# Kernel tuning notes

Measured on AMD Instinct MI355X. Metric: run time of the kernel, lower is better.

Reference implementation:

```python
import jax, jax.numpy as jnp
import numpy as np


def setup_inputs() -> dict:
    key = jax.random.key(0)
    k1, k2, k3 = jax.random.split(key, 3)
    B, C, H, W = 32, 2048, 14, 14
    OUT = 512
    x = jax.random.normal(k1, (B, C, H, W), dtype=jnp.float32)
    gamma = jnp.zeros((1,), dtype=jnp.float32)  # nn.Parameter(torch.zeros(1))
    # 1x1 conv 2048 -> 512 (layer=4 branch), kaiming-ish scale
    conv_w = jax.random.normal(k2, (OUT, C, 1, 1), dtype=jnp.float32) * (1.0 / np.sqrt(C))
    conv_b = jax.random.normal(k3, (OUT,), dtype=jnp.float32) * 0.01
    return {"x": x, "gamma": gamma, "conv_w": conv_w, "conv_b": conv_b}


def reference(x, gamma, conv_w, conv_b):
    B, C, H, W = x.shape
    q = x.reshape(B, C, H * W)                      # [B, C, N]
    # energy[b, c, d] = <q[b,c,:], q[b,d,:]>
    energy = jnp.einsum('bcn,bdn->bcd', q, q)       # [B, C, C]
    # max-subtract trick: softmax(max - energy) along last dim
    energy_new = jnp.max(energy, axis=-1, keepdims=True) - energy
    attention = jax.nn.softmax(energy_new, axis=-1)  # [B, C, C]
    out = jnp.einsum('bcd,bdn->bcn', attention, q).reshape(B, C, H, W)
    out = gamma * out + x
    # 1x1 conv, stride 1, no padding (layer=4 branch)
    pam_out = jax.lax.conv_general_dilated(
        out, conv_w, window_strides=(1, 1), padding='VALID',
        dimension_numbers=('NCHW', 'OIHW', 'NCHW'))
    pam_out = pam_out + conv_b[None, :, None, None]
    return pam_out
```

## Files before the change

kernel.cpp:

```cpp
#include <hip/hip_runtime.h>
#include <hip/hip_bf16.h>
#include <stdint.h>

#define B_   32
#define C_   2048
#define HW_  196
#define OUT_ 512
#define KT_  128
#define MT_  64
#define NKT  (C_ / KT_)

typedef short short8 __attribute__((ext_vector_type(8)));
typedef float floatx4 __attribute__((ext_vector_type(4)));
typedef unsigned short u16;

#define VMCNT_WAIT(n) __builtin_amdgcn_s_waitcnt(0x0F70 | (n))

__device__ __forceinline__ uint32_t pack_bf16(float a, float b) {
  union { __hip_bfloat162 h; uint32_t u; } c;
  c.h = __float22bfloat162_rn(make_float2(a, b));
  return c.u;
}

__device__ __forceinline__ void async_ld16(const u16* g, void* lds_base) {
  __builtin_amdgcn_global_load_lds(
      (const __attribute__((address_space(1))) uint32_t*)g,
      (__attribute__((address_space(3))) uint32_t*)lds_base, 16, 0, 0);
}

__global__ void attn_fallback(const float* __restrict__ x, const float* __restrict__ gamma,
                              float* __restrict__ y) {
  float g = gamma[0];
  if (g == 0.0f) return;
  __shared__ float qc[HW_];
  __shared__ float e[C_];
  __shared__ float red[256];
  int tid = threadIdx.x;
  for (int cRow = blockIdx.x; cRow < C_; cRow += gridDim.x) {
    for (int b = 0; b < B_; ++b) {
      const float* q = x + (size_t)b * C_ * HW_;
      __syncthreads();
      for (int i = tid; i < HW_; i += 256) qc[i] = q[(size_t)cRow * HW_ + i];
      __syncthreads();
      for (int d = tid; d < C_; d += 256) {
        float s = 0.f;
        const float* qd = q + (size_t)d * HW_;
        for (int n = 0; n < HW_; ++n) s += qc[n] * qd[n];
        e[d] = s;
      }
      __syncthreads();
      float mn = 3.4e38f;
      for (int d = tid; d < C_; d += 256) mn = fminf(mn, e[d]);
      red[tid] = mn; __syncthreads();
      for (int s = 128; s > 0; s >>= 1) { if (tid < s) red[tid] = fminf(red[tid], red[tid + s]); __syncthreads(); }
      float emin = red[0];
      __syncthreads();
      float ps = 0.f;
      for (int d = tid; d < C_; d += 256) { float p = __expf(emin - e[d]); e[d] = p; ps += p; }
      red[tid] = ps; __syncthreads();
      for (int s = 128; s > 0; s >>= 1) { if (tid < s) red[tid] += red[tid + s]; __syncthreads(); }
      float S = red[0];
      __syncthreads();
      float invS = 1.f / S;
      for (int n = tid; n < HW_; n += 256) {
        float acc = 0.f;
        for (int d = 0; d < C_; ++d) acc += e[d] * q[(size_t)d * HW_ + n];
        y[((size_t)b * C_ + cRow) * HW_ + n] = g * acc * invS + q[(size_t)cRow * HW_ + n];
      }
    }
  }
}

__global__ __launch_bounds__(256, 3) void xposeW_kernel(
    const float* __restrict__ x, const float* __restrict__ ysrc,
    const float* __restrict__ gamma, u16* __restrict__ xT,
    const float* __restrict__ w, u16* __restrict__ wbf) {
  int tid = threadIdx.x;
  if (blockIdx.x >= 1024) {
    int gid = (blockIdx.x - 1024) * 256 + tid;
    float4 v = ((const float4*)w)[gid];
    ((uint2*)wbf)[gid] = make_uint2(pack_bf16(v.x, v.y), pack_bf16(v.z, v.w));
    return;
  }
  __shared__ float tile[64 * 197];
  const float* src = (gamma[0] != 0.f) ? ysrc : x;
  int b  = blockIdx.x >> 5;
  int c0 = (blockIdx.x & 31) * 64;
  const float* sb = src + ((size_t)b * C_ + c0) * HW_;
  for (int r = 0; r < 13; ++r) {
    int u = r * 256 + tid;
    if (u < 3136) {
      int ci = u / 49, n4 = u - ci * 49;
      float4 v = *(const float4*)(sb + (size_t)ci * HW_ + n4 * 4);
      float* tp = &tile[ci * 197 + n4 * 4];
      tp[0] = v.x; tp[1] = v.y; tp[2] = v.z; tp[3] = v.w;
    }
  }
  __syncthreads();
  u16* xTb = xT + (size_t)b * HW_ * C_ + c0;
  for (int r = 0; r < 7; ++r) {
    int u = r * 256 + tid;
    if (u < 1568) {
      int c8 = u & 7, n = u >> 3;
      const float* tp = &tile[c8 * 8 * 197 + n];
      uint4 o;
      o.x = pack_bf16(tp[0 * 197], tp[1 * 197]);
      o.y = pack_bf16(tp[2 * 197], tp[3 * 197]);
      o.z = pack_bf16(tp[4 * 197], tp[5 * 197]);
      o.w = pack_bf16(tp[6 * 197], tp[7 * 197]);
      *(uint4*)(xTb + (size_t)n * C_ + c8 * 8) = o;
    }
  }
}

template<int P>
__device__ __forceinline__ void gemm_body(
    const u16* __restrict__ xT, const u16* __restrict__ wbf,
    const float* __restrict__ bias, float* __restrict__ out,
    u16* lds0, u16* lds1, int b, int oBase, int n0) {

  int tid  = threadIdx.x;
  int wave = tid >> 6;
  int lane = tid & 63;
  int col  = lane & 15;
  int quad = lane >> 4;

  const u16* xTb  = xT + (size_t)b * HW_ * C_;
  const u16* aPtr = wbf + (size_t)(oBase + wave * 16 + col) * C_;
  int maxRel = HW_ - 1 - n0;

  floatx4 acc[P];
#pragma unroll
  for (int i = 0; i < P; ++i) { floatx4 z = {0.f, 0.f, 0.f, 0.f}; acc[i] = z; }

  const u16* bPtr[P];
  int ldsOff[P];
#pragma unroll
  for (int jj = 0; jj < P; ++jj) {
    int n    = 4 * wave + quad + 16 * jj;
    int srcN = n0 + (n > maxRel ? maxRel : n);
    int kc   = col ^ (4 * wave + quad);
    bPtr[jj]   = xTb + (size_t)srcN * C_ + kc * 8;
    ldsOff[jj] = (wave + 4 * jj) * 512;
  }

  int aK = 0;
  auto issueB = [&](u16* dst) {
#pragma unroll
    for (int jj = 0; jj < P; ++jj) {
      async_ld16(bPtr[jj], dst + ldsOff[jj]);
      bPtr[jj] += KT_;
    }
  };
  uint4 aR[4];
  auto loadA = [&]() {
#pragma unroll
    for (int ks = 0; ks < 4; ++ks)
      aR[ks] = *(const uint4*)(aPtr + aK + ks * 32 + quad * 8);
    aK += KT_;
  };
  auto phase = [&](const u16* buf) {
    __builtin_amdgcn_s_setprio(1);
#pragma unroll
    for (int ks = 0; ks < 4; ++ks) {
      union { uint4 u; short8 v; } af; af.u = aR[ks];
      int chunk = (ks * 4 + quad) ^ col;
      const u16* base = buf + col * KT_ + chunk * 8;
#pragma unroll
      for (int nt = 0; nt < P; ++nt) {
        short8 bf = *(const short8*)(base + nt * 16 * KT_);
        acc[nt] = __builtin_amdgcn_mfma_f32_16x16x32_bf16(af.v, bf, acc[nt], 0, 0, 0);
      }
    }
    __builtin_amdgcn_s_setprio(0);
  };

  issueB(lds0);
  loadA();
  issueB(lds1);
  u16* cur = lds0; u16* nxt = lds1;
#pragma unroll
  for (int kt = 0; kt < NKT - 1; ++kt) {
    VMCNT_WAIT(P);
    __builtin_amdgcn_s_barrier();
    phase(cur);
    loadA();
    __builtin_amdgcn_s_barrier();
    if (kt < NKT - 2) issueB(cur);
    u16* t = cur; cur = nxt; nxt = t;
  }
  VMCNT_WAIT(0);
  __builtin_amdgcn_s_barrier();
  phase(cur);

  int nLim = HW_ - n0; if (nLim > 16 * P) nLim = 16 * P;
  float* outb = out + (size_t)b * OUT_ * HW_;
#pragma unroll
  for (int r = 0; r < 4; ++r) {
    int o = oBase + wave * 16 + quad * 4 + r;
    float bv = bias[o];
    float* orow = outb + (size_t)o * HW_ + n0;
#pragma unroll
    for (int nt = 0; nt < P; ++nt) {
      int nl = nt * 16 + col;
      if (nl < nLim) orow[nl] = acc[nt][r] + bv;
    }
  }
}

__global__ __launch_bounds__(256, 2) void conv_gemm(
    const u16* __restrict__ xT, const u16* __restrict__ wbf,
    const float* __restrict__ bias, float* __restrict__ out) {

  __shared__ __align__(16) u16 Bs2[2][112 * KT_];

  int bid = blockIdx.x;
  int xcd = bid & 7;
  int s   = bid >> 3;
  int ot  = s & 7;
  int g   = ((s >> 3) << 3) | xcd;
  int b   = g >> 1;
  int nh  = g & 1;

  if (nh == 0)
    gemm_body<7>(xT, wbf, bias, out, Bs2[0], Bs2[1], b, ot * MT_, 0);
  else
    gemm_body<6>(xT, wbf, bias, out, Bs2[0], Bs2[1], b, ot * MT_, 112);
}

extern "C" void kernel_launch(void* const* d_in, const int* in_sizes, int n_in,
                              void* d_out, int out_size, void* d_ws, size_t ws_size,
                              hipStream_t stream) {
  const float* x      = (const float*)d_in[0];
  const float* gamma  = (const float*)d_in[1];
  const float* conv_w = (const float*)d_in[2];
  const float* conv_b = (const float*)d_in[3];
  float* out = (float*)d_out;

  const size_t wbf_bytes = (size_t)OUT_ * C_ * sizeof(u16);
  const size_t xT_bytes  = (size_t)B_ * HW_ * C_ * sizeof(u16);
  const size_t y_bytes   = (size_t)B_ * C_ * HW_ * sizeof(float);
  u16*   wbf = (u16*)d_ws;
  u16*   xT  = (u16*)((char*)d_ws + wbf_bytes);
  float* yws = (float*)((char*)d_ws + wbf_bytes + xT_bytes);
  bool have_fallback_ws = ws_size >= wbf_bytes + xT_bytes + y_bytes;
  const float* ysrc = have_fallback_ws ? (const float*)yws : x;

  if (have_fallback_ws)
    attn_fallback<<<dim3(256), dim3(256), 0, stream>>>(x, gamma, yws);
  xposeW_kernel<<<dim3(2048), dim3(256), 0, stream>>>(
      x, ysrc, gamma, xT, conv_w, wbf);
  conv_gemm<<<dim3(512), dim3(256), 0, stream>>>(xT, wbf, conv_b, out);
}
```

Before: 126.2 us.

## Retile conv GEMM to 128 output channels by 64 pixels per block

The 1x1-conv GEMM block tile changes from 64 output channels by 112/84 pixel columns to 128 output channels by 64 pixel columns. Each wave now holds two 16-row A fragments and reuses each LDS B fragment across two MFMAs, which halves LDS reads per MFMA and drops the templated uneven split. The 196 pixels are covered by four 64-wide tiles, the last one overlapping the third. That overlap adds redundant MFMA work and duplicate identical stores, and it raises the A register footprint per wave.

```diff
diff --git a/kernel.cpp b/kernel.cpp
--- a/kernel.cpp
+++ b/kernel.cpp
@@ -7,8 +7,9 @@
 #define HW_  196
 #define OUT_ 512
 #define KT_  128
-#define MT_  64
 #define NKT  (C_ / KT_)
+#define BN_  64
+#define PD_  4
 
 typedef short short8 __attribute__((ext_vector_type(8)));
 typedef float floatx4 __attribute__((ext_vector_type(4)));
@@ -113,11 +114,22 @@
   }
 }
 
-template<int P>
-__device__ __forceinline__ void gemm_body(
+__global__ __launch_bounds__(256, 2) void conv_gemm(
     const u16* __restrict__ xT, const u16* __restrict__ wbf,
-    const float* __restrict__ bias, float* __restrict__ out,
-    u16* lds0, u16* lds1, int b, int oBase, int n0) {
+    const float* __restrict__ bias, float* __restrict__ out) {
+
+  __shared__ __align__(16) u16 Bs2[2][BN_ * KT_];
+
+  int bid = blockIdx.x;
+  int xcd = bid & 7;
+  int s   = bid >> 3;
+  int ot  = s & 3;
+  int gl  = s >> 2;
+  int grp = xcd * 16 + gl;
+  int b   = grp >> 2;
+  int nh  = grp & 3;
+  int n0  = (nh < 3) ? nh * 64 : (HW_ - BN_);
+  int oBase = ot * 128;
 
   int tid  = threadIdx.x;
   int wave = tid >> 6;
@@ -126,62 +138,66 @@
   int quad = lane >> 4;
 
   const u16* xTb  = xT + (size_t)b * HW_ * C_;
-  const u16* aPtr = wbf + (size_t)(oBase + wave * 16 + col) * C_;
-  int maxRel = HW_ - 1 - n0;
-
-  floatx4 acc[P];
-#pragma unroll
-  for (int i = 0; i < P; ++i) { floatx4 z = {0.f, 0.f, 0.f, 0.f}; acc[i] = z; }
-
-  const u16* bPtr[P];
-  int ldsOff[P];
-#pragma unroll
-  for (int jj = 0; jj < P; ++jj) {
-    int n    = 4 * wave + quad + 16 * jj;
-    int srcN = n0 + (n > maxRel ? maxRel : n);
-    int kc   = col ^ (4 * wave + quad);
-    bPtr[jj]   = xTb + (size_t)srcN * C_ + kc * 8;
+  const u16* aPtr = wbf + (size_t)(oBase + wave * 32 + col) * C_ + quad * 8;
+
+  floatx4 acc[2][4];
+#pragma unroll
+  for (int m = 0; m < 2; ++m)
+#pragma unroll
+    for (int nt = 0; nt < 4; ++nt) { floatx4 z = {0.f, 0.f, 0.f, 0.f}; acc[m][nt] = z; }
+
+  const u16* bPtr[PD_];
+  int ldsOff[PD_];
+#pragma unroll
+  for (int jj = 0; jj < PD_; ++jj) {
+    int rl = 4 * wave + quad + 16 * jj;
+    int kc = col ^ (4 * wave + quad);
+    bPtr[jj]   = xTb + (size_t)(n0 + rl) * C_ + kc * 8;
     ldsOff[jj] = (wave + 4 * jj) * 512;
   }
 
+  uint4 aR[8];
   int aK = 0;
+  auto loadA = [&]() {
+#pragma unroll
+    for (int m = 0; m < 2; ++m)
+#pragma unroll
+      for (int ks = 0; ks < 4; ++ks)
+        aR[m * 4 + ks] = *(const uint4*)(aPtr + (size_t)m * 16 * C_ + aK + ks * 32);
+    aK += KT_;
+  };
   auto issueB = [&](u16* dst) {
 #pragma unroll
-    for (int jj = 0; jj < P; ++jj) {
+    for (int jj = 0; jj < PD_; ++jj) {
       async_ld16(bPtr[jj], dst + ldsOff[jj]);
       bPtr[jj] += KT_;
     }
-  };
-  uint4 aR[4];
-  auto loadA = [&]() {
-#pragma unroll
-    for (int ks = 0; ks < 4; ++ks)
-      aR[ks] = *(const uint4*)(aPtr + aK + ks * 32 + quad * 8);
-    aK += KT_;
   };
   auto phase = [&](const u16* buf) {
     __builtin_amdgcn_s_setprio(1);
 #pragma unroll
     for (int ks = 0; ks < 4; ++ks) {
-      union { uint4 u; short8 v; } af; af.u = aR[ks];
+      union { uint4 u; short8 v; } a0, a1;
+      a0.u = aR[ks]; a1.u = aR[4 + ks];
       int chunk = (ks * 4 + quad) ^ col;
       const u16* base = buf + col * KT_ + chunk * 8;
 #pragma unroll
-      for (int nt = 0; nt < P; ++nt) {
+      for (int nt = 0; nt < 4; ++nt) {
         short8 bf = *(const short8*)(base + nt * 16 * KT_);
-        acc[nt] = __builtin_amdgcn_mfma_f32_16x16x32_bf16(af.v, bf, acc[nt], 0, 0, 0);
+        acc[0][nt] = __builtin_amdgcn_mfma_f32_16x16x32_bf16(a0.v, bf, acc[0][nt], 0, 0, 0);
+        acc[1][nt] = __builtin_amdgcn_mfma_f32_16x16x32_bf16(a1.v, bf, acc[1][nt], 0, 0, 0);
       }
     }
     __builtin_amdgcn_s_setprio(0);
   };
 
-  issueB(lds0);
+  issueB(Bs2[0]);
   loadA();
-  issueB(lds1);
-  u16* cur = lds0; u16* nxt = lds1;
+  issueB(Bs2[1]);
+  u16* cur = Bs2[0]; u16* nxt = Bs2[1];
 #pragma unroll
   for (int kt = 0; kt < NKT - 1; ++kt) {
-    VMCNT_WAIT(P);
+    VMCNT_WAIT(PD_);
     __builtin_amdgcn_s_barrier();
     phase(cur);
     loadA();
@@ -193,39 +209,18 @@
   __builtin_amdgcn_s_barrier();
   phase(cur);
 
-  int nLim = HW_ - n0; if (nLim > 16 * P) nLim = 16 * P;
   float* outb = out + (size_t)b * OUT_ * HW_;
 #pragma unroll
-  for (int r = 0; r < 4; ++r) {
-    int o = oBase + wave * 16 + quad * 4 + r;
-    float bv = bias[o];
-    float* orow = outb + (size_t)o * HW_ + n0;
-#pragma unroll
-    for (int nt = 0; nt < P; ++nt) {
-      int nl = nt * 16 + col;
-      if (nl < nLim) orow[nl] = acc[nt][r] + bv;
-    }
-  }
-}
-
-__global__ __launch_bounds__(256, 2) void conv_gemm(
-    const u16* __restrict__ xT, const u16* __restrict__ wbf,
-    const float* __restrict__ bias, float* __restrict__ out) {
-
-  __shared__ __align__(16) u16 Bs2[2][112 * KT_];
-
-  int bid = blockIdx.x;
-  int xcd = bid & 7;
-  int s   = bid >> 3;
-  int ot  = s & 7;
-  int g   = ((s >> 3) << 3) | xcd;
-  int b   = g >> 1;
-  int nh  = g & 1;
-
-  if (nh == 0)
-    gemm_body<7>(xT, wbf, bias, out, Bs2[0], Bs2[1], b, ot * MT_, 0);
-  else
-    gemm_body<6>(xT, wbf, bias, out, Bs2[0], Bs2[1], b, ot * MT_, 112);
+  for (int m = 0; m < 2; ++m)
+#pragma unroll
+    for (int r = 0; r < 4; ++r) {
+      int o = oBase + wave * 32 + m * 16 + quad * 4 + r;
+      float bv = bias[o];
+      float* orow = outb + (size_t)o * HW_ + n0;
+#pragma unroll
+      for (int nt = 0; nt < 4; ++nt)
+        orow[nt * 16 + col] = acc[m][nt][r] + bv;
+    }
 }
 
 extern "C" void kernel_launch(void* const* d_in, const int* in_sizes, int n_in,
```

New measurement: 135.5 us. 1.07x slower.
